# Performance work log

Hardware: AMD Instinct MI355X
Metric: run time of the kernel (lower is better)

The kernel has to match this reference:

```python
import math
import jax, jax.numpy as jnp
import numpy as np

NUM_LEVELS = 3
K = 9          # filter_size
SIGMA = 2.0
OMEGA_X = 0.25
OMEGA_Y = 0.25
C = 64         # channels


def _fan_filter():
    # low-pass Gaussian, shape (C,1,K,K)
    ax = jnp.arange(K, dtype=jnp.float32) - (K - 1) / 2.0
    xx, yy = jnp.meshgrid(ax, ax, indexing='ij')
    lp = jnp.exp(-(xx ** 2 + yy ** 2) / (2.0 * SIGMA ** 2))
    lp = lp / jnp.sum(lp)
    lp = jnp.tile(lp[None, None], (C, 1, 1, 1))
    # high-pass: negate and add delta at center of channel 0 ONLY (faithful to source)
    hp = -lp
    c = K // 2
    hp = hp.at[0, 0, c, c].add(1.0)
    # fan modulation
    cy = jnp.arange(K, dtype=jnp.float32) - K // 2
    cx = jnp.arange(K, dtype=jnp.float32) - K // 2
    y, x = jnp.meshgrid(cy, cx, indexing='ij')
    mod = jnp.cos(2.0 * math.pi * (OMEGA_X * x + OMEGA_Y * y))
    return hp * mod


def _shear_sample(x, s):
    """affine_grid(theta=[[1,s,0],[0,1,0]]) + grid_sample(bilinear, zeros, align_corners=False)."""
    B, Cc, H, W = x.shape
    dt = x.dtype
    # align_corners=False normalized base grid
    xn = (2.0 * jnp.arange(W, dtype=dt) + 1.0) / W - 1.0  # (W,)
    yn = (2.0 * jnp.arange(H, dtype=dt) + 1.0) / H - 1.0  # (H,)
    gx = xn[None, :] + s * yn[:, None]                    # (H,W)
    gy = jnp.broadcast_to(yn[:, None], (H, W))            # (H,W)
    # unnormalize (align_corners=False)
    ix = ((gx + 1.0) * W - 1.0) / 2.0
    iy = ((gy + 1.0) * H - 1.0) / 2.0
    ix0 = jnp.floor(ix); iy0 = jnp.floor(iy)
    ix1 = ix0 + 1.0;     iy1 = iy0 + 1.0
    wx1 = ix - ix0; wx0 = 1.0 - wx1
    wy1 = iy - iy0; wy0 = 1.0 - wy1

    def gather(yi, xi):
        yc = jnp.clip(yi, 0, H - 1).astype(jnp.int32)
        xc = jnp.clip(xi, 0, W - 1).astype(jnp.int32)
        valid = ((yi >= 0) & (yi < H) & (xi >= 0) & (xi < W)).astype(dt)
        return x[:, :, yc, xc] * valid  # (B,C,H,W)

    out = (gather(iy0, ix0) * (wy0 * wx0)
           + gather(iy0, ix1) * (wy0 * wx1)
           + gather(iy1, ix0) * (wy1 * wx0)
           + gather(iy1, ix1) * (wy1 * wx1))
    return out


def _dwconv(x, filt):
    # depthwise cross-correlation, padding K//2 (matches F.conv2d groups=C)
    return jax.lax.conv_general_dilated(
        x, filt, window_strides=(1, 1),
        padding=[(K // 2, K // 2), (K // 2, K // 2)],
        dimension_numbers=('NCHW', 'OIHW', 'NCHW'),
        feature_group_count=C)


def _dfb(x, filt):
    out1 = _dwconv(_shear_sample(x, 1.0), filt)
    out2 = _dwconv(_shear_sample(x, -1.0), filt)
    return out1, out2


def _binary_dfb(x, filt, level):
    if level == 0:
        return [x]
    d1, d2 = _dfb(x, filt)
    return _binary_dfb(d1, filt, level - 1) + _binary_dfb(d2, filt, level - 1)


def setup_inputs() -> dict:
    key = jax.random.key(0)
    x = jax.random.normal(key, (4, C, 256, 256), dtype=jnp.float32)
    filt = _fan_filter()  # buffer (C,1,K,K)
    return {"x": x, "filt": filt}


def reference(x, filt):
    # stack of 2^NUM_LEVELS directional subbands, shape (8, B, C, H, W)
    return jnp.stack(_binary_dfb(x, filt, NUM_LEVELS))
```

## Files before the change

### kernel.cpp

```cpp
#include <hip/hip_runtime.h>
#include <hip/hip_fp16.h>


#define B_ 4
#define C_ 64
#define H_ 256
#define W_ 256
#define TH 32
#define SROWS (TH + 8)
#define SCOLS (W_ + 8)
#define NPB 2048
#define PSTRIDE 260
#define PPLANE (H_ * PSTRIDE)

struct alignas(4) h8 { unsigned int u[4]; };

struct Factors { float A0, A2, A4, A6, A8, B1, B3, B5, B7, vc[9]; };

static __device__ __forceinline__ Factors mk_factors(const float* __restrict__ filt)
{
    const float* f1 = filt + 81;
    Factors F;
    F.A4 = sqrtf(fmaxf(-f1[4 * 9 + 4], 0.f));
    const float rA4 = 1.f / F.A4;
    F.A0 = -f1[0 * 9 + 4] * rA4;  F.A2 = -f1[2 * 9 + 4] * rA4;
    F.A6 = -f1[6 * 9 + 4] * rA4;  F.A8 = -f1[8 * 9 + 4] * rA4;
    F.B5 = sqrtf(fmaxf(f1[5 * 9 + 5], 0.f));
    const float rB5 = 1.f / F.B5;
    F.B1 = f1[1 * 9 + 5] * rB5;  F.B3 = f1[3 * 9 + 5] * rB5;
    F.B7 = f1[7 * 9 + 5] * rB5;
    F.vc[0] = -F.A0; F.vc[1] = F.B1; F.vc[2] = -F.A2; F.vc[3] = F.B3;
    F.vc[4] = -F.A4; F.vc[5] = F.B5; F.vc[6] = -F.A6; F.vc[7] = F.B7;
    F.vc[8] = -F.A8;
    return F;
}

static __device__ __forceinline__ float4 shear_avg_h(const h8 raw, int d)
{
    union { h8 r; __half2 h2[4]; } U; U.r = raw;
    const bool qhi   = (d & 1) != 0;
    const bool valid = (unsigned)d < 260u;
    const float2 g01 = __half22float2(U.h2[0]);
    const float2 g23 = __half22float2(U.h2[1]);
    const float2 g45 = __half22float2(U.h2[2]);
    const float t0 = qhi ? g01.y : g01.x;
    const float t1 = qhi ? g23.x : g01.y;
    const float t2 = qhi ? g23.y : g23.x;
    const float t3 = qhi ? g45.x : g23.y;
    const float t4 = qhi ? g45.y : g45.x;
    float4 v;
    v.x = valid ? 0.5f * (t0 + t1) : 0.f;
    v.y = valid ? 0.5f * (t1 + t2) : 0.f;
    v.z = valid ? 0.5f * (t2 + t3) : 0.f;
    v.w = valid ? 0.5f * (t3 + t4) : 0.f;
    return v;
}

template<bool DST_H>
static __device__ __forceinline__ void compute_store(
    float (&s_sh)[SROWS][SCOLS], void* __restrict__ dst_, const Factors& F,
    int plane_idx, int c, int h0t, bool first_pad)
{
    const int tid  = threadIdx.x;
    const int rg   = tid >> 6;
    const int lane = tid & 63;
    const int w0   = lane * 4;

    float acc[8][4];
    #pragma unroll
    for (int i = 0; i < 8; ++i)
        #pragma unroll
        for (int j = 0; j < 4; ++j) acc[i][j] = 0.f;

    __builtin_amdgcn_s_setprio(1);
    #pragma unroll
    for (int t = 0; t < 16; ++t) {
        const int rr = rg * 8 + t;
        const float4 sa  = *(const float4*)&s_sh[rr][w0];
        const float4 sb  = *(const float4*)&s_sh[rr][w0 + 4];
        const float4 sc4 = *(const float4*)&s_sh[rr][w0 + 8];
        const float s[12] = {sa.x, sa.y, sa.z, sa.w,
                             sb.x, sb.y, sb.z, sb.w,
                             sc4.x, sc4.y, sc4.z, sc4.w};
        float ha[4], hb[4];
        #pragma unroll
        for (int j = 0; j < 4; ++j) {
            ha[j] = fmaf(F.A8, s[j + 8],
                    fmaf(F.A6, s[j + 6],
                    fmaf(F.A4, s[j + 4],
                    fmaf(F.A2, s[j + 2], F.A0 * s[j]))));
            hb[j] = fmaf(F.B7, s[j + 7],
                    fmaf(F.B5, s[j + 5],
                    fmaf(F.B3, s[j + 3], F.B1 * s[j + 1])));
        }
        #pragma unroll
        for (int i = 0; i < 8; ++i) {
            const int ky = t - i;
            if (ky >= 0 && ky < 9) {
                #pragma unroll
                for (int j = 0; j < 4; ++j) {
                    const float hv = (ky & 1) ? hb[j] : ha[j];
                    acc[i][j] = fmaf(F.vc[ky], hv, acc[i][j]);
                }
            }
        }
    }
    __builtin_amdgcn_s_setprio(0);

    if (c == 0) {
        #pragma unroll
        for (int i = 0; i < 8; ++i) {
            const float4 sv = *(const float4*)&s_sh[rg * 8 + i + 4][w0 + 4];
            acc[i][0] += sv.x; acc[i][1] += sv.y; acc[i][2] += sv.z; acc[i][3] += sv.w;
        }
    }

    if (DST_H) {
        __half* plane = (__half*)dst_ + (size_t)plane_idx * PPLANE;
        if (lane < 8) {
            uint2 z; z.x = 0u; z.y = 0u;
            *(uint2*)(plane + (size_t)(h0t + rg * 8 + lane + 1) * PSTRIDE) = z;
        }
        if (first_pad && tid == 8) {
            uint2 z; z.x = 0u; z.y = 0u;
            *(uint2*)dst_ = z;
        }
        __half* optr = plane + (size_t)(h0t + rg * 8) * PSTRIDE + 4 + (lane * 4);
        #pragma unroll
        for (int i = 0; i < 8; ++i) {
            union { __half2 h2; unsigned int u; } p0, p1;
            p0.h2 = __floats2half2_rn(acc[i][0], acc[i][1]);
            p1.h2 = __floats2half2_rn(acc[i][2], acc[i][3]);
            uint2 pk; pk.x = p0.u; pk.y = p1.u;
            *(uint2*)(optr + (size_t)i * PSTRIDE) = pk;
        }
    } else {
        float* optr = (float*)dst_
            + (((size_t)plane_idx) * H_ + h0t + rg * 8) * (size_t)W_ + (lane * 4);
        #pragma unroll
        for (int i = 0; i < 8; ++i) {
            const float4 v = {acc[i][0], acc[i][1], acc[i][2], acc[i][3]};
            *(float4*)(optr + (size_t)i * W_) = v;
        }
    }
}

template<bool DST_H>
__global__ __launch_bounds__(256) void shear_pair_kernel(
    const void* __restrict__ in_, void* __restrict__ dst0_,
    void* __restrict__ dst1_, const float* __restrict__ filt)
{
    __shared__ float s_sh[SROWS][SCOLS];

    const int tid  = threadIdx.x;
    const int bid  = (int)blockIdx.x;
    const int tile = bid & 7;
    const int c    = (bid >> 3) & 63;
    const int b    = bid >> 9;
    const int h0   = tile * TH;
    const int wave = tid >> 6;
    const int lane = tid & 63;
    const int plane_idx = b * C_ + c;
    const __half* src = (const __half*)in_ + (size_t)plane_idx * PPLANE;

    if (tid < 80) {
        const int r = tid >> 1;
        *(float4*)&s_sh[r][(tid & 1) ? 260 : 0] = make_float4(0.f, 0.f, 0.f, 0.f);
    }

    #pragma unroll
    for (int u = 0; u < 10; ++u) {
        const int r  = wave + u * 4;
        const int hr = h0 + r - 4;
        float4 v = make_float4(0.f, 0.f, 0.f, 0.f);
        if ((unsigned)hr < 256u) {
            const __half* rowh = src + (size_t)hr * PSTRIDE;
            const int d  = -128 + hr + 4 + lane * 4;
            const int mc = min(max(d & ~1, 0), 258);
            const h8 raw = *(const h8*)(rowh + mc);
            v = shear_avg_h(raw, d);
        }
        *(float4*)&s_sh[r][4 + lane * 4] = v;
    }

    h8 R[10] = {};
    #pragma unroll
    for (int u = 0; u < 10; ++u) {
        const int hr = h0 + wave + u * 4 - 4;
        if ((unsigned)hr < 256u) {
            const __half* rowh = src + (size_t)hr * PSTRIDE;
            const int d  = 127 - hr + 4 + lane * 4;
            const int mc = min(max(d & ~1, 0), 258);
            R[u] = *(const h8*)(rowh + mc);
        }
    }
    __builtin_amdgcn_sched_barrier(0);

    const Factors F = mk_factors(filt);

    __syncthreads();
    compute_store<DST_H>(s_sh, dst0_, F, plane_idx, c, h0, bid == 0);
    __syncthreads();

    #pragma unroll
    for (int u = 0; u < 10; ++u) {
        const int r  = wave + u * 4;
        const int hr = h0 + r - 4;
        float4 v = make_float4(0.f, 0.f, 0.f, 0.f);
        if ((unsigned)hr < 256u) {
            const int d = 127 - hr + 4 + lane * 4;
            v = shear_avg_h(R[u], d);
        }
        *(float4*)&s_sh[r][4 + lane * 4] = v;
    }
    __syncthreads();
    compute_store<DST_H>(s_sh, dst1_, F, plane_idx, c, h0, bid == 0);
}

__global__ __launch_bounds__(256) void shear_x_kernel(
    const float* __restrict__ in, void* __restrict__ dst_,
    const float* __restrict__ filt, int parity)
{
    __shared__ float s_sh[SROWS][SCOLS];

    const int tid  = threadIdx.x;
    const int bid  = (int)blockIdx.x;
    const int tile = bid & 7;
    const int c    = (bid >> 3) & 63;
    const int b    = bid >> 9;
    const int h0   = tile * TH;
    const int sign = parity ? -1 : 1;
    const int off  = parity ? 127 : -128;
    const int plane_idx = b * C_ + c;

    {
        const int wave = tid >> 6;
        const int lane = tid & 63;

        if (tid < 80) {
            const int r = tid >> 1;
            *(float4*)&s_sh[r][(tid & 1) ? 260 : 0] = make_float4(0.f, 0.f, 0.f, 0.f);
        }

        #pragma unroll
        for (int u = 0; u < 10; ++u) {
            const int r  = wave + u * 4;
            const int hr = h0 + r - 4;
            float4 v = make_float4(0.f, 0.f, 0.f, 0.f);
            if ((unsigned)hr < 256u) {
                const float* row = in + (size_t)plane_idx * (H_ * W_)
                                      + (size_t)hr * W_;
                const int c0 = off + sign * hr + lane * 4;
                float t0 = row[min(max(c0,     0), 255)];
                float t1 = row[min(max(c0 + 1, 0), 255)];
                float t2 = row[min(max(c0 + 2, 0), 255)];
                float t3 = row[min(max(c0 + 3, 0), 255)];
                float t4 = row[min(max(c0 + 4, 0), 255)];
                t0 = ((unsigned)c0       < 256u) ? t0 : 0.f;
                t1 = ((unsigned)(c0 + 1) < 256u) ? t1 : 0.f;
                t2 = ((unsigned)(c0 + 2) < 256u) ? t2 : 0.f;
                t3 = ((unsigned)(c0 + 3) < 256u) ? t3 : 0.f;
                t4 = ((unsigned)(c0 + 4) < 256u) ? t4 : 0.f;
                v.x = 0.5f * (t0 + t1);
                v.y = 0.5f * (t1 + t2);
                v.z = 0.5f * (t2 + t3);
                v.w = 0.5f * (t3 + t4);
            }
            *(float4*)&s_sh[r][4 + lane * 4] = v;
        }
    }

    const Factors F = mk_factors(filt);
    __syncthreads();
    compute_store<true>(s_sh, dst_, F, plane_idx, c, h0, bid == 0);
}

extern "C" void kernel_launch(void* const* d_in, const int* in_sizes, int n_in,
                              void* d_out, int out_size, void* d_ws, size_t ws_size,
                              hipStream_t stream) {
    const float* x    = (const float*)d_in[0];
    const float* filt = (const float*)d_in[1];
    float* out = (float*)d_out;
    void*  wsb = d_ws;
    const size_t N = (size_t)B_ * C_ * H_ * W_;

    float* S[8];
    for (int k = 0; k < 8; ++k) S[k] = out + (size_t)k * N;

    void* Bh  = (void*)S[0];
    void* BAh = (void*)S[2];
    void* BBh = (void*)S[3];
    void* Ah  = (void*)S[1];
    void* AAh = (void*)S[2];
    void* ABh = wsb;

    const dim3 block(256);
    const dim3 grid(NPB);

    #define LX(src, dst, par) \
        shear_x_kernel<<<grid, block, 0, stream>>>(src, dst, filt, par)
    #define P(DH, src, d0, d1) \
        shear_pair_kernel<DH><<<grid, block, 0, stream>>>(src, d0, d1, filt)

    LX(x, Bh, 1);
    P(true , Bh,  BAh,  BBh );
    P(false, BAh, S[4], S[5]);
    P(false, BBh, S[6], S[7]);
    LX(x, Ah, 0);
    P(true , Ah,  AAh,  ABh );
    P(false, AAh, S[0], S[1]);
    P(false, ABh, S[2], S[3]);
    #undef LX
    #undef P
}
```

Measured before the change: 367.7 us.

## Fuse level-1 shear pair from x and batch two level-3 pair launches

Replaces the two separate shear_x launches on x with a single shear_xpair kernel that reads each x tile once and produces both shear directions, keeping the second direction's taps in registers. It also merges two independent level-3 pair launches into one grid of twice the size, and reassigns the intermediate buffers inside the output to fit the new order. The aim is to cut redundant reads of x, reduce launch count and improve occupancy at the tail of each launch, at the cost of more registers (50 floats per thread) and heavier buffer aliasing.

After: 361.9 us. About the same (-1.6%).

```diff
diff --git a/kernel.cpp b/kernel.cpp
--- a/kernel.cpp
+++ b/kernel.cpp
@@ -146,8 +146,98 @@
 }
 
 template<bool DST_H>
+static __device__ __forceinline__ void pair_body(
+    const void* __restrict__ in_, void* __restrict__ dst0_,
+    void* __restrict__ dst1_, const float* __restrict__ filt, int inner)
+{
+    __shared__ float s_sh[SROWS][SCOLS];
+
+    const int tid  = threadIdx.x;
+    const int tile = inner & 7;
+    const int c    = (inner >> 3) & 63;
+    const int b    = inner >> 9;
+    const int h0   = tile * TH;
+    const int wave = tid >> 6;
+    const int lane = tid & 63;
+    const int plane_idx = b * C_ + c;
+    const __half* src = (const __half*)in_ + (size_t)plane_idx * PPLANE;
+
+    if (tid < 80) {
+        const int r = tid >> 1;
+        *(float4*)&s_sh[r][(tid & 1) ? 260 : 0] = make_float4(0.f, 0.f, 0.f, 0.f);
+    }
+
+    #pragma unroll
+    for (int u = 0; u < 10; ++u) {
+        const int r  = wave + u * 4;
+        const int hr = h0 + r - 4;
+        float4 v = make_float4(0.f, 0.f, 0.f, 0.f);
+        if ((unsigned)hr < 256u) {
+            const __half* rowh = src + (size_t)hr * PSTRIDE;
+            const int d  = -128 + hr + 4 + lane * 4;
+            const int mc = min(max(d & ~1, 0), 258);
+            const h8 raw = *(const h8*)(rowh + mc);
+            v = shear_avg_h(raw, d);
+        }
+        *(float4*)&s_sh[r][4 + lane * 4] = v;
+    }
+
+    h8 R[10] = {};
+    #pragma unroll
+    for (int u = 0; u < 10; ++u) {
+        const int hr = h0 + wave + u * 4 - 4;
+        if ((unsigned)hr < 256u) {
+            const __half* rowh = src + (size_t)hr * PSTRIDE;
+            const int d  = 127 - hr + 4 + lane * 4;
+            const int mc = min(max(d & ~1, 0), 258);
+            R[u] = *(const h8*)(rowh + mc);
+        }
+    }
+    __builtin_amdgcn_sched_barrier(0);
+
+    const Factors F = mk_factors(filt);
+
+    __syncthreads();
+    compute_store<DST_H>(s_sh, dst0_, F, plane_idx, c, h0, inner == 0);
+    __syncthreads();
+
+    #pragma unroll
+    for (int u = 0; u < 10; ++u) {
+        const int r  = wave + u * 4;
+        const int hr = h0 + r - 4;
+        float4 v = make_float4(0.f, 0.f, 0.f, 0.f);
+        if ((unsigned)hr < 256u) {
+            const int d = 127 - hr + 4 + lane * 4;
+            v = shear_avg_h(R[u], d);
+        }
+        *(float4*)&s_sh[r][4 + lane * 4] = v;
+    }
+    __syncthreads();
+    compute_store<DST_H>(s_sh, dst1_, F, plane_idx, c, h0, inner == 0);
+}
+
+template<bool DST_H>
 __global__ __launch_bounds__(256) void shear_pair_kernel(
     const void* __restrict__ in_, void* __restrict__ dst0_,
+    void* __restrict__ dst1_, const float* __restrict__ filt)
+{
+    pair_body<DST_H>(in_, dst0_, dst1_, filt, (int)blockIdx.x);
+}
+
+__global__ __launch_bounds__(256) void shear_pair4_kernel(
+    const void* __restrict__ s0, const void* __restrict__ s1,
+    void* __restrict__ d00, void* __restrict__ d01,
+    void* __restrict__ d10, void* __restrict__ d11,
+    const float* __restrict__ filt)
+{
+    const int bid   = (int)blockIdx.x;
+    const int k     = bid >> 11;
+    const int inner = bid & 2047;
+    pair_body<false>(k ? s1 : s0, k ? d10 : d00, k ? d11 : d01, filt, inner);
+}
+
+__global__ __launch_bounds__(256) void shear_xpair_kernel(
+    const float* __restrict__ in, void* __restrict__ dst0_,
     void* __restrict__ dst1_, const float* __restrict__ filt)
 {
     __shared__ float s_sh[SROWS][SCOLS];
@@ -161,7 +251,7 @@
     const int wave = tid >> 6;
     const int lane = tid & 63;
     const int plane_idx = b * C_ + c;
-    const __half* src = (const __half*)in_ + (size_t)plane_idx * PPLANE;
+    const float* plane = in + (size_t)plane_idx * (H_ * W_);
 
     if (tid < 80) {
         const int r = tid >> 1;
@@ -174,24 +264,40 @@
         const int hr = h0 + r - 4;
         float4 v = make_float4(0.f, 0.f, 0.f, 0.f);
         if ((unsigned)hr < 256u) {
-            const __half* rowh = src + (size_t)hr * PSTRIDE;
-            const int d  = -128 + hr + 4 + lane * 4;
-            const int mc = min(max(d & ~1, 0), 258);
-            const h8 raw = *(const h8*)(rowh + mc);
-            v = shear_avg_h(raw, d);
+            const float* row = plane + (size_t)hr * W_;
+            const int c0 = -128 + hr + lane * 4;
+            float t0 = row[min(max(c0,     0), 255)];
+            float t1 = row[min(max(c0 + 1, 0), 255)];
+            float t2 = row[min(max(c0 + 2, 0), 255)];
+            float t3 = row[min(max(c0 + 3, 0), 255)];
+            float t4 = row[min(max(c0 + 4, 0), 255)];
+            t0 = ((unsigned)c0       < 256u) ? t0 : 0.f;
+            t1 = ((unsigned)(c0 + 1) < 256u) ? t1 : 0.f;
+            t2 = ((unsigned)(c0 + 2) < 256u) ? t2 : 0.f;
+            t3 = ((unsigned)(c0 + 3) < 256u) ? t3 : 0.f;
+            t4 = ((unsigned)(c0 + 4) < 256u) ? t4 : 0.f;
+            v.x = 0.5f * (t0 + t1);
+            v.y = 0.5f * (t1 + t2);
+            v.z = 0.5f * (t2 + t3);
+            v.w = 0.5f * (t3 + t4);
         }
         *(float4*)&s_sh[r][4 + lane * 4] = v;
     }
 
-    h8 R[10] = {};
-    #pragma unroll
-    for (int u = 0; u < 10; ++u) {
+    float Ra[10][5];
+    #pragma unroll
+    for (int u = 0; u < 10; ++u) {
+        #pragma unroll
+        for (int q = 0; q < 5; ++q) Ra[u][q] = 0.f;
         const int hr = h0 + wave + u * 4 - 4;
         if ((unsigned)hr < 256u) {
-            const __half* rowh = src + (size_t)hr * PSTRIDE;
-            const int d  = 127 - hr + 4 + lane * 4;
-            const int mc = min(max(d & ~1, 0), 258);
-            R[u] = *(const h8*)(rowh + mc);
+            const float* row = plane + (size_t)hr * W_;
+            const int c0 = 127 - hr + lane * 4;
+            Ra[u][0] = row[min(max(c0,     0), 255)];
+            Ra[u][1] = row[min(max(c0 + 1, 0), 255)];
+            Ra[u][2] = row[min(max(c0 + 2, 0), 255)];
+            Ra[u][3] = row[min(max(c0 + 3, 0), 255)];
+            Ra[u][4] = row[min(max(c0 + 4, 0), 255)];
         }
     }
     __builtin_amdgcn_sched_barrier(0);
@@ -199,7 +305,7 @@
     const Factors F = mk_factors(filt);
 
     __syncthreads();
-    compute_store<DST_H>(s_sh, dst0_, F, plane_idx, c, h0, bid == 0);
+    compute_store<true>(s_sh, dst0_, F, plane_idx, c, h0, bid == 0);
     __syncthreads();
 
     #pragma unroll
@@ -208,71 +314,21 @@
         const int hr = h0 + r - 4;
         float4 v = make_float4(0.f, 0.f, 0.f, 0.f);
         if ((unsigned)hr < 256u) {
-            const int d = 127 - hr + 4 + lane * 4;
-            v = shear_avg_h(R[u], d);
+            const int c0 = 127 - hr + lane * 4;
+            const float t0 = ((unsigned)c0       < 256u) ? Ra[u][0] : 0.f;
+            const float t1 = ((unsigned)(c0 + 1) < 256u) ? Ra[u][1] : 0.f;
+            const float t2 = ((unsigned)(c0 + 2) < 256u) ? Ra[u][2] : 0.f;
+            const float t3 = ((unsigned)(c0 + 3) < 256u) ? Ra[u][3] : 0.f;
+            const float t4 = ((unsigned)(c0 + 4) < 256u) ? Ra[u][4] : 0.f;
+            v.x = 0.5f * (t0 + t1);
+            v.y = 0.5f * (t1 + t2);
+            v.z = 0.5f * (t2 + t3);
+            v.w = 0.5f * (t3 + t4);
         }
         *(float4*)&s_sh[r][4 + lane * 4] = v;
     }
     __syncthreads();
-    compute_store<DST_H>(s_sh, dst1_, F, plane_idx, c, h0, bid == 0);
-}
-
-__global__ __launch_bounds__(256) void shear_x_kernel(
-    const float* __restrict__ in, void* __restrict__ dst_,
-    const float* __restrict__ filt, int parity)
-{
-    __shared__ float s_sh[SROWS][SCOLS];
-
-    const int tid  = threadIdx.x;
-    const int bid  = (int)blockIdx.x;
-    const int tile = bid & 7;
-    const int c    = (bid >> 3) & 63;
-    const int b    = bid >> 9;
-    const int h0   = tile * TH;
-    const int sign = parity ? -1 : 1;
-    const int off  = parity ? 127 : -128;
-    const int plane_idx = b * C_ + c;
-
-    {
-        const int wave = tid >> 6;
-        const int lane = tid & 63;
-
-        if (tid < 80) {
-            const int r = tid >> 1;
-            *(float4*)&s_sh[r][(tid & 1) ? 260 : 0] = make_float4(0.f, 0.f, 0.f, 0.f);
-        }
-
-        #pragma unroll
-        for (int u = 0; u < 10; ++u) {
-            const int r  = wave + u * 4;
-            const int hr = h0 + r - 4;
-            float4 v = make_float4(0.f, 0.f, 0.f, 0.f);
-            if ((unsigned)hr < 256u) {
-                const float* row = in + (size_t)plane_idx * (H_ * W_)
-                                      + (size_t)hr * W_;
-                const int c0 = off + sign * hr + lane * 4;
-                float t0 = row[min(max(c0,     0), 255)];
-                float t1 = row[min(max(c0 + 1, 0), 255)];
-                float t2 = row[min(max(c0 + 2, 0), 255)];
-                float t3 = row[min(max(c0 + 3, 0), 255)];
-                float t4 = row[min(max(c0 + 4, 0), 255)];
-                t0 = ((unsigned)c0       < 256u) ? t0 : 0.f;
-                t1 = ((unsigned)(c0 + 1) < 256u) ? t1 : 0.f;
-                t2 = ((unsigned)(c0 + 2) < 256u) ? t2 : 0.f;
-                t3 = ((unsigned)(c0 + 3) < 256u) ? t3 : 0.f;
-                t4 = ((unsigned)(c0 + 4) < 256u) ? t4 : 0.f;
-                v.x = 0.5f * (t0 + t1);
-                v.y = 0.5f * (t1 + t2);
-                v.z = 0.5f * (t2 + t3);
-                v.w = 0.5f * (t3 + t4);
-            }
-            *(float4*)&s_sh[r][4 + lane * 4] = v;
-        }
-    }
-
-    const Factors F = mk_factors(filt);
-    __syncthreads();
-    compute_store<true>(s_sh, dst_, F, plane_idx, c, h0, bid == 0);
+    compute_store<true>(s_sh, dst1_, F, plane_idx, c, h0, bid == 0);
 }
 
 extern "C" void kernel_launch(void* const* d_in, const int* in_sizes, int n_in,
@@ -287,29 +343,24 @@
     float* S[8];
     for (int k = 0; k < 8; ++k) S[k] = out + (size_t)k * N;
 
+    void* Ah  = (void*)S[3];
     void* Bh  = (void*)S[0];
-    void* BAh = (void*)S[2];
-    void* BBh = (void*)S[3];
-    void* Ah  = (void*)S[1];
+    void* BAh = (void*)S[1];
+    void* BBh = (void*)S[2];
     void* AAh = (void*)S[2];
     void* ABh = wsb;
 
     const dim3 block(256);
     const dim3 grid(NPB);
-
-    #define LX(src, dst, par) \
-        shear_x_kernel<<<grid, block, 0, stream>>>(src, dst, filt, par)
-    #define P(DH, src, d0, d1) \
-        shear_pair_kernel<DH><<<grid, block, 0, stream>>>(src, d0, d1, filt)
-
-    LX(x, Bh, 1);
-    P(true , Bh,  BAh,  BBh );
-    P(false, BAh, S[4], S[5]);
-    P(false, BBh, S[6], S[7]);
-    LX(x, Ah, 0);
-    P(true , Ah,  AAh,  ABh );
-    P(false, AAh, S[0], S[1]);
-    P(false, ABh, S[2], S[3]);
-    #undef LX
-    #undef P
-}
+    const dim3 grid4(2 * NPB);
+
+    shear_xpair_kernel<<<grid, block, 0, stream>>>(x, Ah, Bh, filt);
+    shear_pair_kernel<true><<<grid, block, 0, stream>>>(Bh, BAh, BBh, filt);
+    shear_pair4_kernel<<<grid4, block, 0, stream>>>(
+        BAh, BBh, (void*)S[4], (void*)S[5], (void*)S[6], (void*)S[7], filt);
+    shear_pair_kernel<true><<<grid, block, 0, stream>>>(Ah, AAh, ABh, filt);
+    shear_pair_kernel<false><<<grid, block, 0, stream>>>(AAh, (void*)S[0],
+                                                         (void*)S[1], filt);
+    shear_pair_kernel<false><<<grid, block, 0, stream>>>(ABh, (void*)S[2],
+                                                         (void*)S[3], filt);
+}
```
